# Optimization experiments

Hardware: AMD Instinct MI355X
Metric: run time of the kernel (lower is better)

The kernel has to match this reference:

```python
import jax, jax.numpy as jnp
import numpy as np


def _mlp(h, W1, b1, W2, b2):
    # Linear -> ReLU -> Linear
    h = jax.nn.relu(h @ W1 + b1)
    return h @ W2 + b2


def setup_inputs() -> dict:
    key = jax.random.key(0)
    ks = jax.random.split(key, 8)
    N, E, DN, DE, H, O = 50000, 800000, 128, 64, 256, 128
    DIN = DN + DE  # 192
    s1 = 1.0 / np.sqrt(DIN)
    s2 = 1.0 / np.sqrt(H)
    return {
        "x": jax.random.normal(ks[0], (N, DN), dtype=jnp.float32),
        "edge_index": jax.random.randint(ks[1], (2, E), 0, N, dtype=jnp.int32),
        "edge_attr": jax.random.normal(ks[2], (E, DE), dtype=jnp.float32),
        "W1_out": jax.random.normal(ks[3], (DIN, H), dtype=jnp.float32) * s1,
        "b1_out": jnp.zeros((H,), dtype=jnp.float32),
        "W2_out": jax.random.normal(ks[4], (H, O), dtype=jnp.float32) * s2,
        "b2_out": jnp.zeros((O,), dtype=jnp.float32),
        "W1_in": jax.random.normal(ks[5], (DIN, H), dtype=jnp.float32) * s1,
        "b1_in": jnp.zeros((H,), dtype=jnp.float32),
        "W2_in": jax.random.normal(ks[6], (H, O), dtype=jnp.float32) * s2,
        "b2_in": jnp.zeros((O,), dtype=jnp.float32),
    }


def reference(x, edge_index, edge_attr, W1_out, b1_out, W2_out, b2_out,
              W1_in, b1_in, W2_in, b2_in):
    N = x.shape[0]
    row, col = edge_index[0], edge_index[1]
    # Shared gather + concat: [E, d_node + d_edge]
    msg_in = jnp.concatenate([x[col], edge_attr], axis=1)

    # flow_out: edges with row < col. Compute MLP densely, zero masked edges,
    # then scatter-sum -> identical math to masked gather + scatter-sum.
    m_out = (row < col).astype(x.dtype)[:, None]
    flow_out = _mlp(msg_in, W1_out, b1_out, W2_out, b2_out) * m_out
    flow_out = jax.ops.segment_sum(flow_out, row, num_segments=N)

    # flow_in: edges with row > col
    m_in = (row > col).astype(x.dtype)[:, None]
    flow_in = _mlp(msg_in, W1_in, b1_in, W2_in, b2_in) * m_in
    flow_in = jax.ops.segment_sum(flow_in, row, num_segments=N)

    return jnp.concatenate((flow_in, flow_out), axis=1)  # [N, 2*O]
```

## Files before the change

### kernel.cpp

```cpp
#include <hip/hip_runtime.h>
#include <hip/hip_bf16.h>

typedef __attribute__((ext_vector_type(8))) short short8;
typedef __attribute__((ext_vector_type(8))) unsigned short ushort8;
typedef __attribute__((ext_vector_type(4))) float f32x4;
typedef __attribute__((ext_vector_type(2))) unsigned int uint2v;
typedef __attribute__((ext_vector_type(4))) unsigned int uint4v;

#define DN   128
#define DE   64
#define DIN  192
#define HID  256
#define OUTD 128
#define TE   64
#define NT   256
#define MSG_LD 200
#define OUT_LD 132
#define NMB  (TE / 16)

static __device__ __forceinline__ unsigned short f2b(float f) {
    unsigned int u = __float_as_uint(f);
    u += 0x7fffu + ((u >> 16) & 1u);
    return (unsigned short)(u >> 16);
}

static __device__ __forceinline__ unsigned int cvt_pk2(float lo, float hi) {
    unsigned int r;
    asm("v_cvt_pk_bf16_f32 %0, %1, %2" : "=v"(r) : "v"(lo), "v"(hi));
    return r;
}

template<int OFF>
static __device__ __forceinline__ uint2v tr_read(unsigned addr) {
    uint2v d;
    asm volatile("ds_read_b64_tr_b16 %0, %1 offset:%c2"
                 : "=v"(d) : "v"(addr), "n"(OFF));
    return d;
}

__global__ __launch_bounds__(256)
void prep_kernel(const float* __restrict__ W1o, const float* __restrict__ W1i,
                 const float* __restrict__ W2o, const float* __restrict__ W2i,
                 unsigned short* __restrict__ W1po, unsigned short* __restrict__ W1pi,
                 unsigned short* __restrict__ W2po, unsigned short* __restrict__ W2pi,
                 const int* __restrict__ ei, int E, int N, int* __restrict__ hist,
                 const float* __restrict__ x, unsigned short* __restrict__ xb) {
    const int S1 = DIN * HID, S2v = HID * OUTD;
    const int PACKN = 2 * S1 + 2 * S2v;
    int idx = blockIdx.x * blockDim.x + threadIdx.x;
    if (idx < PACKN) {
        const float* W; unsigned short* Wp; int Nc, j;
        if      (idx < S1)          { W = W1o; Wp = W1po; Nc = HID;  j = idx; }
        else if (idx < 2*S1)        { W = W1i; Wp = W1pi; Nc = HID;  j = idx - S1; }
        else if (idx < 2*S1 + S2v)  { W = W2o; Wp = W2po; Nc = OUTD; j = idx - 2*S1; }
        else                        { W = W2i; Wp = W2pi; Nc = OUTD; j = idx - 2*S1 - S2v; }
        int k = j / Nc, n = j - k * Nc;
        Wp[(((k >> 5) * Nc + n) << 5) + (k & 31)] = f2b(W[j]);
    } else if (idx < PACKN + E) {
        int e = idx - PACKN;
        int r = ei[e], c = ei[E + e];
        if      (r < c) atomicAdd(&hist[r], 1);
        else if (r > c) atomicAdd(&hist[N + r], 1);
    } else {
        int i = idx - PACKN - E;
        if (i < N * DN / 8) {
            float4 a = reinterpret_cast<const float4*>(x)[i * 2];
            float4 b = reinterpret_cast<const float4*>(x)[i * 2 + 1];
            ushort8 v = { f2b(a.x), f2b(a.y), f2b(a.z), f2b(a.w),
                          f2b(b.x), f2b(b.y), f2b(b.z), f2b(b.w) };
            reinterpret_cast<ushort8*>(xb)[i] = v;
        }
    }
}

__global__ __launch_bounds__(1024)
void scan1_kernel(const int* __restrict__ hist, int* __restrict__ cursor,
                  int* __restrict__ chunkSum, int N, int nch) {
    __shared__ int s_ws[16];
    const int br = blockIdx.x / nch, ch = blockIdx.x - br * nch;
    const int tid = threadIdx.x, lane = tid & 63, wv = tid >> 6;
    const int i = ch * 1024 + tid;
    int v = (i < N) ? hist[(size_t)br * N + i] : 0;
    int incl = v;
    #pragma unroll
    for (int d = 1; d < 64; d <<= 1) {
        int t = __shfl_up(incl, d, 64);
        if (lane >= d) incl += t;
    }
    if (lane == 63) s_ws[wv] = incl;
    __syncthreads();
    if (tid < 16) {
        int w = s_ws[tid];
        int wi = w;
        #pragma unroll
        for (int d = 1; d < 16; d <<= 1) {
            int t = __shfl_up(wi, d, 64);
            if (tid >= d) wi += t;
        }
        s_ws[tid] = wi - w;
    }
    __syncthreads();
    int excl = s_ws[wv] + incl - v;
    if (i < N) cursor[(size_t)br * N + i] = excl;
    if (tid == 1023) chunkSum[br * nch + ch] = excl + v;
}

__global__ __launch_bounds__(128)
void scan2_kernel(int* __restrict__ chunkSum, int* __restrict__ cnt, int nch) {
    const int br = threadIdx.x >> 6, lane = threadIdx.x & 63;
    int v = (lane < nch) ? chunkSum[br * nch + lane] : 0;
    int incl = v;
    #pragma unroll
    for (int d = 1; d < 64; d <<= 1) {
        int t = __shfl_up(incl, d, 64);
        if (lane >= d) incl += t;
    }
    if (lane < nch) chunkSum[br * nch + lane] = incl - v;
    if (lane == nch - 1) cnt[br] = incl;
}

__global__ __launch_bounds__(256)
void reorder_kernel(const int* __restrict__ ei, int E, int N, int nch,
                    int* __restrict__ cursor, const int* __restrict__ chunkSum,
                    int* __restrict__ list_out, int* __restrict__ list_in) {
    int e = blockIdx.x * blockDim.x + threadIdx.x;
    if (e >= E) return;
    int r = ei[e], c = ei[E + e];
    if (r == c) return;
    int br = (r < c) ? 0 : 1;
    int p = chunkSum[br * nch + (r >> 10)] + atomicAdd(&cursor[(size_t)br * N + r], 1);
    (br ? list_in : list_out)[p] = e;
}

__global__ __launch_bounds__(NT, 4)
void mlp_scatter_kernel(const unsigned short* __restrict__ xb,
                        const int* __restrict__ ei,
                        const float* __restrict__ ea,
                        const unsigned short* __restrict__ W1p_out,
                        const unsigned short* __restrict__ W1p_in,
                        const float* __restrict__ b1_out,
                        const float* __restrict__ b1_in,
                        const unsigned short* __restrict__ W2p_out,
                        const unsigned short* __restrict__ W2p_in,
                        const float* __restrict__ b2_out,
                        const float* __restrict__ b2_in,
                        const int* __restrict__ list_out,
                        const int* __restrict__ list_in,
                        const int* __restrict__ cnt,
                        float* __restrict__ out,
                        int E) {
    __shared__ __align__(16) unsigned short s_buf[TE * 264];
    __shared__ int s_eid[TE], s_dest[TE], s_col[TE];

    const int c0 = cnt[0], c1 = cnt[1];
    const int nb0 = (c0 + TE - 1) / TE;
    const int branch = (blockIdx.x >= nb0) ? 1 : 0;
    const int lb = branch ? (blockIdx.x - nb0) : blockIdx.x;
    const int count = branch ? c1 : c0;
    if (lb * TE >= count) return;
    const int* list            = branch ? list_in : list_out;
    const unsigned short* W1p  = branch ? W1p_in  : W1p_out;
    const float* b1            = branch ? b1_in   : b1_out;
    const unsigned short* W2p  = branch ? W2p_in  : W2p_out;
    const float* b2            = branch ? b2_in   : b2_out;
    const int colbase          = branch ? 0 : OUTD;

    const int tid = threadIdx.x;
    if (tid < TE) {
        int idx = lb * TE + tid;
        int e = (idx < count) ? list[idx] : -1;
        s_eid[tid]  = e;
        s_dest[tid] = (e >= 0) ? ei[e] : -1;
        s_col[tid]  = (e >= 0) ? ei[E + e] : 0;
    }
    __syncthreads();

    {
        const int le  = tid >> 2;
        const int sub = tid & 3;
        const int e   = s_eid[le];
        const ushort8* xrow = reinterpret_cast<const ushort8*>(xb) + (size_t)s_col[le] * (DN / 8);
        #pragma unroll
        for (int j = 0; j < 4; ++j) {
            int seg = sub + j * 4;
            ushort8 v = {0, 0, 0, 0, 0, 0, 0, 0};
            if (e >= 0) v = xrow[seg];
            *reinterpret_cast<ushort8*>(&s_buf[le * MSG_LD + seg * 8]) = v;
        }
        const float4* erow = reinterpret_cast<const float4*>(ea) + (size_t)e * (DE / 4);
        #pragma unroll
        for (int j = 0; j < 4; ++j) {
            float4 v = make_float4(0.f, 0.f, 0.f, 0.f);
            if (e >= 0) v = erow[sub * 4 + j];
            unsigned int lo = cvt_pk2(v.x, v.y);
            unsigned int hi = cvt_pk2(v.z, v.w);
            *reinterpret_cast<uint2*>(&s_buf[le * MSG_LD + DN + sub * 16 + j * 4]) = make_uint2(lo, hi);
        }
    }
    __syncthreads();

    const int wave = tid >> 6;
    const int lane = tid & 63;
    const int ln   = lane & 15;
    const int quad = lane >> 4;

    f32x4 acc[4][4];
    {
        const int nbase = wave * 64;
        float bias[4];
        #pragma unroll
        for (int t = 0; t < 4; ++t) bias[t] = b1[nbase + t * 16 + ln];
        #pragma unroll
        for (int mt = 0; mt < 4; ++mt)
            #pragma unroll
            for (int t = 0; t < 4; ++t)
                acc[mt][t] = (f32x4){bias[t], bias[t], bias[t], bias[t]};
        #pragma unroll
        for (int kt = 0; kt < DIN / 32; ++kt) {
            short8 a[4], b[4];
            #pragma unroll
            for (int mt = 0; mt < 4; ++mt)
                a[mt] = *reinterpret_cast<const short8*>(
                    &s_buf[(mt * 16 + ln) * MSG_LD + kt * 32 + quad * 8]);
            #pragma unroll
            for (int t = 0; t < 4; ++t)
                b[t] = *reinterpret_cast<const short8*>(
                    &W1p[((kt * HID + nbase + t * 16 + ln) << 5) + quad * 8]);
            #pragma unroll
            for (int mt = 0; mt < 4; ++mt)
                #pragma unroll
                for (int t = 0; t < 4; ++t)
                    acc[mt][t] = __builtin_amdgcn_mfma_f32_16x16x32_bf16(a[mt], b[t], acc[mt][t], 0, 0, 0);
        }
    }
    __syncthreads();

    {
        const int nbase = wave * 64;
        #pragma unroll
        for (int mt = 0; mt < 4; ++mt)
            #pragma unroll
            for (int t = 0; t < 4; ++t) {
                int n = nbase + t * 16 + ln;
                float r0 = acc[mt][t][0], r1 = acc[mt][t][1];
                float r2 = acc[mt][t][2], r3 = acc[mt][t][3];
                r0 = r0 > 0.f ? r0 : 0.f;  r1 = r1 > 0.f ? r1 : 0.f;
                r2 = r2 > 0.f ? r2 : 0.f;  r3 = r3 > 0.f ? r3 : 0.f;
                unsigned int d0 = cvt_pk2(r0, r1);
                unsigned int d1 = cvt_pk2(r2, r3);
                int el = (((n >> 2) * NMB + mt) << 6) + ((n & 3) << 4) + (quad << 2);
                *reinterpret_cast<uint2v*>(&s_buf[el]) = (uint2v){d0, d1};
            }
    }
    __syncthreads();

    f32x4 acc2[4][2];
    {
        const int nb2 = wave * 32;
        float bz0 = b2[nb2 + ln];
        float bz1 = b2[nb2 + 16 + ln];
        #pragma unroll
        for (int mt = 0; mt < 4; ++mt) {
            acc2[mt][0] = (f32x4){bz0, bz0, bz0, bz0};
            acc2[mt][1] = (f32x4){bz1, bz1, bz1, bz1};
        }
        const unsigned trb = (unsigned)(uintptr_t)(&s_buf[quad * 512 + ln * 4]);
        short8 bn0 = *reinterpret_cast<const short8*>(&W2p[((nb2 + ln) << 5) + quad * 8]);
        short8 bn1 = *reinterpret_cast<const short8*>(&W2p[((nb2 + 16 + ln) << 5) + quad * 8]);

#define G2TR(kt, mt) { \
        uint2v t0 = tr_read<(kt) * 4096 + (mt) * 128>(trb); \
        uint2v t1 = tr_read<(kt) * 4096 + (mt) * 128 + 512>(trb); \
        a[mt] = __builtin_bit_cast(short8, (uint4v){t0.x, t0.y, t1.x, t1.y}); }

#define G2MM(mt) \
        acc2[mt][0] = __builtin_amdgcn_mfma_f32_16x16x32_bf16(a[mt], b0c, acc2[mt][0], 0, 0, 0); \
        acc2[mt][1] = __builtin_amdgcn_mfma_f32_16x16x32_bf16(a[mt], b1c, acc2[mt][1], 0, 0, 0);

#define G2STEP(kt) { \
        short8 a[4]; \
        G2TR(kt, 0) G2TR(kt, 1) G2TR(kt, 2) G2TR(kt, 3) \
        short8 b0c = bn0, b1c = bn1; \
        if ((kt) < 7) { \
            bn0 = *reinterpret_cast<const short8*>(&W2p[((((kt) + 1) * OUTD + nb2 + ln) << 5) + quad * 8]); \
            bn1 = *reinterpret_cast<const short8*>(&W2p[((((kt) + 1) * OUTD + nb2 + 16 + ln) << 5) + quad * 8]); \
        } \
        asm volatile("s_waitcnt lgkmcnt(0)"); \
        __builtin_amdgcn_sched_barrier(0); \
        G2MM(0) G2MM(1) G2MM(2) G2MM(3) }

        G2STEP(0) G2STEP(1) G2STEP(2) G2STEP(3)
        G2STEP(4) G2STEP(5) G2STEP(6) G2STEP(7)
#undef G2STEP
#undef G2MM
#undef G2TR
    }
    __syncthreads();

    float* s_outf = reinterpret_cast<float*>(s_buf);
    {
        const int nb2 = wave * 32;
        #pragma unroll
        for (int mt = 0; mt < 4; ++mt)
            #pragma unroll
            for (int t = 0; t < 2; ++t)
                #pragma unroll
                for (int r = 0; r < 4; ++r)
                    s_outf[(mt * 16 + quad * 4 + r) * OUT_LD + nb2 + t * 16 + ln] = acc2[mt][t][r];
    }
    __syncthreads();

    {
        const int c  = tid & 127;
        const int m0 = (tid >> 7) * 32;
        float run = 0.f;
        int cur = -1, rs = m0;
        for (int m = m0; m < m0 + 32; ++m) {
            int d = s_dest[m];
            float v = s_outf[m * OUT_LD + c];
            if (d != cur) {
                if (cur >= 0) {
                    float* p = &out[(size_t)cur * (2 * OUTD) + colbase + c];
                    if (rs > m0) *p = run; else atomicAdd(p, run);
                }
                cur = d; run = 0.f; rs = m;
            }
            if (d >= 0) run += v;
        }
        if (cur >= 0)
            atomicAdd(&out[(size_t)cur * (2 * OUTD) + colbase + c], run);
    }
}

extern "C" void kernel_launch(void* const* d_in, const int* in_sizes, int n_in,
                              void* d_out, int out_size, void* d_ws, size_t ws_size,
                              hipStream_t stream) {
    const float* x   = (const float*)d_in[0];
    const int*   ei  = (const int*)d_in[1];
    const float* ea  = (const float*)d_in[2];
    const float* W1o = (const float*)d_in[3];
    const float* b1o = (const float*)d_in[4];
    const float* W2o = (const float*)d_in[5];
    const float* b2o = (const float*)d_in[6];
    const float* W1i = (const float*)d_in[7];
    const float* b1i = (const float*)d_in[8];
    const float* W2i = (const float*)d_in[9];
    const float* b2i = (const float*)d_in[10];
    float* out = (float*)d_out;
    const int E = in_sizes[1] / 2;
    const int N = in_sizes[0] / DN;
    const int nch = (N + 1023) >> 10;

    int* cnt      = (int*)d_ws;
    int* chunkSum = cnt + 16;
    int* hist     = chunkSum + 128;
    int* cursor   = hist + 2 * (size_t)N;
    int* list_out = cursor + 2 * (size_t)N;
    int* list_in  = list_out + E;
    unsigned short* W1po = (unsigned short*)(list_in + E);
    unsigned short* W1pi = W1po + DIN * HID;
    unsigned short* W2po = W1pi + DIN * HID;
    unsigned short* W2pi = W2po + HID * OUTD;
    unsigned short* xb   = W2pi + HID * OUTD;

    hipMemsetAsync(d_out, 0, (size_t)out_size * sizeof(float), stream);
    hipMemsetAsync(d_ws, 0, (576 + 8 * (size_t)N), stream);

    const int PACKN = 2 * DIN * HID + 2 * HID * OUTD;
    const int prepN = PACKN + E + N * DN / 8;
    prep_kernel<<<(prepN + 255) / 256, 256, 0, stream>>>(
        W1o, W1i, W2o, W2i, W1po, W1pi, W2po, W2pi, ei, E, N, hist, x, xb);

    scan1_kernel<<<2 * nch, 1024, 0, stream>>>(hist, cursor, chunkSum, N, nch);
    scan2_kernel<<<1, 128, 0, stream>>>(chunkSum, cnt, nch);
    reorder_kernel<<<(E + 255) / 256, 256, 0, stream>>>(
        ei, E, N, nch, cursor, chunkSum, list_out, list_in);

    const int nblk = (E + TE - 1) / TE + 2;
    mlp_scatter_kernel<<<nblk, NT, 0, stream>>>(
        xb, ei, ea, W1po, W1pi, b1o, b1i, W2po, W2pi, b2o, b2i,
        list_out, list_in, cnt, out, E);
}
```

Baseline: 573.7 us.

## Precompute per-node first-layer projection and gather it instead of raw node features

Result: slower. 622.2 us (+8.5%).

```diff
diff --git a/kernel.cpp b/kernel.cpp
--- a/kernel.cpp
+++ b/kernel.cpp
@@ -14,7 +14,9 @@
 #define OUTD 128
 #define TE   64
 #define NT   256
-#define MSG_LD 200
+#define EA_LD 72
+#define Z_LD  264
+#define ZX_LD 136
 #define OUT_LD 132
 #define NMB  (TE / 16)
 
@@ -43,8 +45,7 @@
                  const float* __restrict__ W2o, const float* __restrict__ W2i,
                  unsigned short* __restrict__ W1po, unsigned short* __restrict__ W1pi,
                  unsigned short* __restrict__ W2po, unsigned short* __restrict__ W2pi,
-                 const int* __restrict__ ei, int E, int N, int* __restrict__ hist,
-                 const float* __restrict__ x, unsigned short* __restrict__ xb) {
+                 const int* __restrict__ ei, int E, int N, int* __restrict__ hist) {
     const int S1 = DIN * HID, S2v = HID * OUTD;
     const int PACKN = 2 * S1 + 2 * S2v;
     int idx = blockIdx.x * blockDim.x + threadIdx.x;
@@ -61,14 +62,92 @@
         int r = ei[e], c = ei[E + e];
         if      (r < c) atomicAdd(&hist[r], 1);
         else if (r > c) atomicAdd(&hist[N + r], 1);
-    } else {
-        int i = idx - PACKN - E;
-        if (i < N * DN / 8) {
-            float4 a = reinterpret_cast<const float4*>(x)[i * 2];
-            float4 b = reinterpret_cast<const float4*>(x)[i * 2 + 1];
-            ushort8 v = { f2b(a.x), f2b(a.y), f2b(a.z), f2b(a.w),
-                          f2b(b.x), f2b(b.y), f2b(b.z), f2b(b.w) };
-            reinterpret_cast<ushort8*>(xb)[i] = v;
+    }
+}
+
+__global__ __launch_bounds__(256, 4)
+void z_kernel(const float* __restrict__ x,
+              const unsigned short* __restrict__ W1p_out,
+              const unsigned short* __restrict__ W1p_in,
+              const float* __restrict__ b1_out, const float* __restrict__ b1_in,
+              unsigned short* __restrict__ z, int N) {
+    __shared__ __align__(16) unsigned short s_t[64 * Z_LD];
+    const int nzb = (N + 63) >> 6;
+    const int branch = (blockIdx.x >= nzb) ? 1 : 0;
+    const int zb = blockIdx.x - branch * nzb;
+    const unsigned short* W1p = branch ? W1p_in : W1p_out;
+    const float* b1           = branch ? b1_in  : b1_out;
+    const int r0 = zb * 64;
+    const int tid = threadIdx.x;
+
+    {
+        const int row = tid >> 2, sub = tid & 3;
+        const float* xr = x + (size_t)(r0 + row) * DN + sub * 32;
+        const bool ok = (r0 + row) < N;
+        #pragma unroll
+        for (int j = 0; j < 4; ++j) {
+            float4 a = make_float4(0.f, 0.f, 0.f, 0.f), b = a;
+            if (ok) {
+                a = *reinterpret_cast<const float4*>(xr + j * 8);
+                b = *reinterpret_cast<const float4*>(xr + j * 8 + 4);
+            }
+            uint4v v = { cvt_pk2(a.x, a.y), cvt_pk2(a.z, a.w),
+                         cvt_pk2(b.x, b.y), cvt_pk2(b.z, b.w) };
+            *reinterpret_cast<uint4v*>(&s_t[row * ZX_LD + sub * 32 + j * 8]) = v;
+        }
+    }
+    __syncthreads();
+
+    const int wave = tid >> 6, lane = tid & 63, ln = lane & 15, quad = lane >> 4;
+    const int nbase = wave * 64;
+    f32x4 acc[4][4];
+    {
+        float bias[4];
+        #pragma unroll
+        for (int t = 0; t < 4; ++t) bias[t] = b1[nbase + t * 16 + ln];
+        #pragma unroll
+        for (int mt = 0; mt < 4; ++mt)
+            #pragma unroll
+            for (int t = 0; t < 4; ++t)
+                acc[mt][t] = (f32x4){bias[t], bias[t], bias[t], bias[t]};
+        #pragma unroll
+        for (int kt = 0; kt < DN / 32; ++kt) {
+            short8 a[4], b[4];
+            #pragma unroll
+            for (int mt = 0; mt < 4; ++mt)
+                a[mt] = *reinterpret_cast<const short8*>(
+                    &s_t[(mt * 16 + ln) * ZX_LD + kt * 32 + quad * 8]);
+            #pragma unroll
+            for (int t = 0; t < 4; ++t)
+                b[t] = *reinterpret_cast<const short8*>(
+                    &W1p[((kt * HID + nbase + t * 16 + ln) << 5) + quad * 8]);
+            #pragma unroll
+            for (int mt = 0; mt < 4; ++mt)
+                #pragma unroll
+                for (int t = 0; t < 4; ++t)
+                    acc[mt][t] = __builtin_amdgcn_mfma_f32_16x16x32_bf16(a[mt], b[t], acc[mt][t], 0, 0, 0);
+        }
+    }
+    __syncthreads();
+
+    #pragma unroll
+    for (int mt = 0; mt < 4; ++mt)
+        #pragma unroll
+        for (int t = 0; t < 4; ++t) {
+            int n = nbase + t * 16 + ln;
+            #pragma unroll
+            for (int r = 0; r < 4; ++r)
+                s_t[(mt * 16 + quad * 4 + r) * Z_LD + n] = f2b(acc[mt][t][r]);
+        }
+    __syncthreads();
+
+    {
+        unsigned short* zg = z + (size_t)branch * N * HID;
+        for (int c = tid; c < 64 * 32; c += NT) {
+            int row = c >> 5, ch = c & 31;
+            if (r0 + row < N)
+                reinterpret_cast<ushort8*>(zg + (size_t)(r0 + row) * HID)[ch] =
+                    *reinterpret_cast<const ushort8*>(&s_t[row * Z_LD + ch * 8]);
         }
     }
 }
@@ -132,14 +211,12 @@
     (br ? list_in : list_out)[p] = e;
 }
 
-__global__ __launch_bounds__(NT, 4)
-void mlp_scatter_kernel(const unsigned short* __restrict__ xb,
+__global__ __launch_bounds__(NT, 3)
+void mlp_scatter_kernel(const unsigned short* __restrict__ z,
                         const int* __restrict__ ei,
                         const float* __restrict__ ea,
                         const unsigned short* __restrict__ W1p_out,
                         const unsigned short* __restrict__ W1p_in,
-                        const float* __restrict__ b1_out,
-                        const float* __restrict__ b1_in,
                         const unsigned short* __restrict__ W2p_out,
                         const unsigned short* __restrict__ W2p_in,
                         const float* __restrict__ b2_out,
@@ -148,8 +225,9 @@
                         const int* __restrict__ list_in,
                         const int* __restrict__ cnt,
                         float* __restrict__ out,
-                        int E) {
-    __shared__ __align__(16) unsigned short s_buf[TE * 264];
+                        int E, int N) {
+    __shared__ __align__(16) unsigned short s_buf[TE * Z_LD];
+    __shared__ __align__(16) unsigned short s_msg[TE * EA_LD];
     __shared__ int s_eid[TE], s_dest[TE], s_col[TE];
 
     const int c0 = cnt[0], c1 = cnt[1];
@@ -160,7 +238,6 @@
     if (lb * TE >= count) return;
     const int* list            = branch ? list_in : list_out;
     const unsigned short* W1p  = branch ? W1p_in  : W1p_out;
-    const float* b1            = branch ? b1_in   : b1_out;
     const unsigned short* W2p  = branch ? W2p_in  : W2p_out;
     const float* b2            = branch ? b2_in   : b2_out;
     const int colbase          = branch ? 0 : OUTD;
@@ -179,13 +256,14 @@
         const int le  = tid >> 2;
         const int sub = tid & 3;
         const int e   = s_eid[le];
-        const ushort8* xrow = reinterpret_cast<const ushort8*>(xb) + (size_t)s_col[le] * (DN / 8);
-        #pragma unroll
-        for (int j = 0; j < 4; ++j) {
-            int seg = sub + j * 4;
+        const ushort8* zrow = reinterpret_cast<const ushort8*>(z)
+            + ((size_t)branch * N + s_col[le]) * (HID / 8);
+        #pragma unroll
+        for (int j = 0; j < 8; ++j) {
+            int seg = j * 4 + sub;
             ushort8 v = {0, 0, 0, 0, 0, 0, 0, 0};
-            if (e >= 0) v = xrow[seg];
-            *reinterpret_cast<ushort8*>(&s_buf[le * MSG_LD + seg * 8]) = v;
+            if (e >= 0) v = zrow[seg];
+            *reinterpret_cast<ushort8*>(&s_buf[le * Z_LD + seg * 8]) = v;
         }
         const float4* erow = reinterpret_cast<const float4*>(ea) + (size_t)e * (DE / 4);
         #pragma unroll
@@ -194,7 +272,7 @@
             if (e >= 0) v = erow[sub * 4 + j];
             unsigned int lo = cvt_pk2(v.x, v.y);
             unsigned int hi = cvt_pk2(v.z, v.w);
-            *reinterpret_cast<uint2*>(&s_buf[le * MSG_LD + DN + sub * 16 + j * 4]) = make_uint2(lo, hi);
+            *reinterpret_cast<uint2*>(&s_msg[le * EA_LD + sub * 16 + j * 4]) = make_uint2(lo, hi);
         }
     }
     __syncthreads();
@@ -207,25 +285,29 @@
     f32x4 acc[4][4];
     {
         const int nbase = wave * 64;
-        float bias[4];
-        #pragma unroll
-        for (int t = 0; t < 4; ++t) bias[t] = b1[nbase + t * 16 + ln];
         #pragma unroll
         for (int mt = 0; mt < 4; ++mt)
             #pragma unroll
-            for (int t = 0; t < 4; ++t)
-                acc[mt][t] = (f32x4){bias[t], bias[t], bias[t], bias[t]};
-        #pragma unroll
-        for (int kt = 0; kt < DIN / 32; ++kt) {
+            for (int t = 0; t < 4; ++t) {
+                int n = nbase + t * 16 + ln;
+                #pragma unroll
+                for (int r = 0; r < 4; ++r) {
+                    int m = mt * 16 + quad * 4 + r;
+                    acc[mt][t][r] = __uint_as_float(
+                        (unsigned int)s_buf[m * Z_LD + n] << 16);
+                }
+            }
+        #pragma unroll
+        for (int kt = 0; kt < DE / 32; ++kt) {
             short8 a[4], b[4];
             #pragma unroll
             for (int mt = 0; mt < 4; ++mt)
                 a[mt] = *reinterpret_cast<const short8*>(
-                    &s_buf[(mt * 16 + ln) * MSG_LD + kt * 32 + quad * 8]);
+                    &s_msg[(mt * 16 + ln) * EA_LD + kt * 32 + quad * 8]);
             #pragma unroll
             for (int t = 0; t < 4; ++t)
                 b[t] = *reinterpret_cast<const short8*>(
-                    &W1p[((kt * HID + nbase + t * 16 + ln) << 5) + quad * 8]);
+                    &W1p[(((kt + DN / 32) * HID + nbase + t * 16 + ln) << 5) + quad * 8]);
             #pragma unroll
             for (int mt = 0; mt < 4; ++mt)
                 #pragma unroll
@@ -361,15 +443,23 @@
     unsigned short* W1pi = W1po + DIN * HID;
     unsigned short* W2po = W1pi + DIN * HID;
     unsigned short* W2pi = W2po + HID * OUTD;
-    unsigned short* xb   = W2pi + HID * OUTD;
+    unsigned short* zws  = W2pi + HID * OUTD;
+
+    size_t need = (size_t)(144 + 4 * (size_t)N + 2 * (size_t)E) * 4
+                + (size_t)(2 * DIN * HID + 2 * HID * OUTD) * 2
+                + (size_t)2 * N * HID * 2;
+    if (need > ws_size) return;
 
     hipMemsetAsync(d_out, 0, (size_t)out_size * sizeof(float), stream);
     hipMemsetAsync(d_ws, 0, (576 + 8 * (size_t)N), stream);
 
     const int PACKN = 2 * DIN * HID + 2 * HID * OUTD;
-    const int prepN = PACKN + E + N * DN / 8;
+    const int prepN = PACKN + E;
     prep_kernel<<<(prepN + 255) / 256, 256, 0, stream>>>(
-        W1o, W1i, W2o, W2i, W1po, W1pi, W2po, W2pi, ei, E, N, hist, x, xb);
+        W1o, W1i, W2o, W2i, W1po, W1pi, W2po, W2pi, ei, E, N, hist);
+
+    const int nzb = (N + 63) >> 6;
+    z_kernel<<<2 * nzb, 256, 0, stream>>>(x, W1po, W1pi, b1o, b1i, zws, N);
 
     scan1_kernel<<<2 * nch, 1024, 0, stream>>>(hist, cursor, chunkSum, N, nch);
     scan2_kernel<<<1, 128, 0, stream>>>(chunkSum, cnt, nch);
@@ -378,6 +468,6 @@
 
     const int nblk = (E + TE - 1) / TE + 2;
     mlp_scatter_kernel<<<nblk, NT, 0, stream>>>(
-        xb, ei, ea, W1po, W1pi, b1o, b1i, W2po, W2pi, b2o, b2i,
-        list_out, list_in, cnt, out, E);
-}
+        zws, ei, ea, W1po, W1pi, W2po, W2pi, b2o, b2i,
+        list_out, list_in, cnt, out, E, N);
+}
```

## Load x operands directly from global, overlap edge_attr staging, double-buffer GEMM2 reads

Applied to the files above, without the earlier changes.

Result: slower. 627.0 us (+9.3%).

```diff
diff --git a/kernel.cpp b/kernel.cpp
--- a/kernel.cpp
+++ b/kernel.cpp
@@ -14,7 +14,7 @@
 #define OUTD 128
 #define TE   64
 #define NT   256
-#define MSG_LD 200
+#define EA_LD 72
 #define OUT_LD 132
 #define NMB  (TE / 16)
 
@@ -175,35 +175,22 @@
     }
     __syncthreads();
 
-    {
-        const int le  = tid >> 2;
-        const int sub = tid & 3;
-        const int e   = s_eid[le];
-        const ushort8* xrow = reinterpret_cast<const ushort8*>(xb) + (size_t)s_col[le] * (DN / 8);
-        #pragma unroll
-        for (int j = 0; j < 4; ++j) {
-            int seg = sub + j * 4;
-            ushort8 v = {0, 0, 0, 0, 0, 0, 0, 0};
-            if (e >= 0) v = xrow[seg];
-            *reinterpret_cast<ushort8*>(&s_buf[le * MSG_LD + seg * 8]) = v;
-        }
-        const float4* erow = reinterpret_cast<const float4*>(ea) + (size_t)e * (DE / 4);
-        #pragma unroll
-        for (int j = 0; j < 4; ++j) {
-            float4 v = make_float4(0.f, 0.f, 0.f, 0.f);
-            if (e >= 0) v = erow[sub * 4 + j];
-            unsigned int lo = cvt_pk2(v.x, v.y);
-            unsigned int hi = cvt_pk2(v.z, v.w);
-            *reinterpret_cast<uint2*>(&s_buf[le * MSG_LD + DN + sub * 16 + j * 4]) = make_uint2(lo, hi);
-        }
-    }
-    __syncthreads();
-
     const int wave = tid >> 6;
     const int lane = tid & 63;
     const int ln   = lane & 15;
     const int quad = lane >> 4;
 
+    const int le  = tid >> 2;
+    const int sub = tid & 3;
+    const int eg  = s_eid[le];
+    float4 ev[4];
+    {
+        const float4* erow = reinterpret_cast<const float4*>(ea)
+            + (size_t)(eg < 0 ? 0 : eg) * (DE / 4);
+        #pragma unroll
+        for (int j = 0; j < 4; ++j) ev[j] = erow[sub * 4 + j];
+    }
+
     f32x4 acc[4][4];
     {
         const int nbase = wave * 64;
@@ -215,17 +202,53 @@
             #pragma unroll
             for (int t = 0; t < 4; ++t)
                 acc[mt][t] = (f32x4){bias[t], bias[t], bias[t], bias[t]};
-        #pragma unroll
-        for (int kt = 0; kt < DIN / 32; ++kt) {
+
+        const unsigned short* xp0 = xb + (size_t)s_col[0 * 16 + ln] * DN + quad * 8;
+        const unsigned short* xp1 = xb + (size_t)s_col[1 * 16 + ln] * DN + quad * 8;
+        const unsigned short* xp2 = xb + (size_t)s_col[2 * 16 + ln] * DN + quad * 8;
+        const unsigned short* xp3 = xb + (size_t)s_col[3 * 16 + ln] * DN + quad * 8;
+        #pragma unroll
+        for (int kt = 0; kt < DN / 32; ++kt) {
             short8 a[4], b[4];
-            #pragma unroll
-            for (int mt = 0; mt < 4; ++mt)
-                a[mt] = *reinterpret_cast<const short8*>(
-                    &s_buf[(mt * 16 + ln) * MSG_LD + kt * 32 + quad * 8]);
+            a[0] = *reinterpret_cast<const short8*>(xp0 + kt * 32);
+            a[1] = *reinterpret_cast<const short8*>(xp1 + kt * 32);
+            a[2] = *reinterpret_cast<const short8*>(xp2 + kt * 32);
+            a[3] = *reinterpret_cast<const short8*>(xp3 + kt * 32);
             #pragma unroll
             for (int t = 0; t < 4; ++t)
                 b[t] = *reinterpret_cast<const short8*>(
                     &W1p[((kt * HID + nbase + t * 16 + ln) << 5) + quad * 8]);
+            #pragma unroll
+            for (int mt = 0; mt < 4; ++mt)
+                #pragma unroll
+                for (int t = 0; t < 4; ++t)
+                    acc[mt][t] = __builtin_amdgcn_mfma_f32_16x16x32_bf16(a[mt], b[t], acc[mt][t], 0, 0, 0);
+        }
+    }
+
+    {
+        #pragma unroll
+        for (int j = 0; j < 4; ++j) {
+            unsigned int lo = cvt_pk2(ev[j].x, ev[j].y);
+            unsigned int hi = cvt_pk2(ev[j].z, ev[j].w);
+            *reinterpret_cast<uint2*>(&s_buf[le * EA_LD + sub * 16 + j * 4]) = make_uint2(lo, hi);
+        }
+    }
+    __syncthreads();
+
+    {
+        const int nbase = wave * 64;
+        #pragma unroll
+        for (int kk = 0; kk < DE / 32; ++kk) {
+            short8 a[4], b[4];
+            #pragma unroll
+            for (int mt = 0; mt < 4; ++mt)
+                a[mt] = *reinterpret_cast<const short8*>(
+                    &s_buf[(mt * 16 + ln) * EA_LD + kk * 32 + quad * 8]);
+            #pragma unroll
+            for (int t = 0; t < 4; ++t)
+                b[t] = *reinterpret_cast<const short8*>(
+                    &W1p[(((kk + DN / 32) * HID + nbase + t * 16 + ln) << 5) + quad * 8]);
             #pragma unroll
             for (int mt = 0; mt < 4; ++mt)
                 #pragma unroll
@@ -268,32 +291,52 @@
         short8 bn0 = *reinterpret_cast<const short8*>(&W2p[((nb2 + ln) << 5) + quad * 8]);
         short8 bn1 = *reinterpret_cast<const short8*>(&W2p[((nb2 + 16 + ln) << 5) + quad * 8]);
 
-#define G2TR(kt, mt) { \
-        uint2v t0 = tr_read<(kt) * 4096 + (mt) * 128>(trb); \
-        uint2v t1 = tr_read<(kt) * 4096 + (mt) * 128 + 512>(trb); \
-        a[mt] = __builtin_bit_cast(short8, (uint4v){t0.x, t0.y, t1.x, t1.y}); }
-
-#define G2MM(mt) \
-        acc2[mt][0] = __builtin_amdgcn_mfma_f32_16x16x32_bf16(a[mt], b0c, acc2[mt][0], 0, 0, 0); \
-        acc2[mt][1] = __builtin_amdgcn_mfma_f32_16x16x32_bf16(a[mt], b1c, acc2[mt][1], 0, 0, 0);
-
-#define G2STEP(kt) { \
-        short8 a[4]; \
-        G2TR(kt, 0) G2TR(kt, 1) G2TR(kt, 2) G2TR(kt, 3) \
+#define G2LOAD(dst, kt) { \
+        uint2v u0 = tr_read<(kt) * 4096 + 0 * 128>(trb); \
+        uint2v u1 = tr_read<(kt) * 4096 + 0 * 128 + 512>(trb); \
+        uint2v u2 = tr_read<(kt) * 4096 + 1 * 128>(trb); \
+        uint2v u3 = tr_read<(kt) * 4096 + 1 * 128 + 512>(trb); \
+        uint2v u4 = tr_read<(kt) * 4096 + 2 * 128>(trb); \
+        uint2v u5 = tr_read<(kt) * 4096 + 2 * 128 + 512>(trb); \
+        uint2v u6 = tr_read<(kt) * 4096 + 3 * 128>(trb); \
+        uint2v u7 = tr_read<(kt) * 4096 + 3 * 128 + 512>(trb); \
+        dst[0] = __builtin_bit_cast(short8, (uint4v){u0.x, u0.y, u1.x, u1.y}); \
+        dst[1] = __builtin_bit_cast(short8, (uint4v){u2.x, u2.y, u3.x, u3.y}); \
+        dst[2] = __builtin_bit_cast(short8, (uint4v){u4.x, u4.y, u5.x, u5.y}); \
+        dst[3] = __builtin_bit_cast(short8, (uint4v){u6.x, u6.y, u7.x, u7.y}); }
+
+#define G2WAIT8 { asm volatile("s_waitcnt lgkmcnt(8)"); __builtin_amdgcn_sched_barrier(0); }
+#define G2WAIT0 { asm volatile("s_waitcnt lgkmcnt(0)"); __builtin_amdgcn_sched_barrier(0); }
+
+#define G2MMA(src, kt) { \
         short8 b0c = bn0, b1c = bn1; \
         if ((kt) < 7) { \
             bn0 = *reinterpret_cast<const short8*>(&W2p[((((kt) + 1) * OUTD + nb2 + ln) << 5) + quad * 8]); \
             bn1 = *reinterpret_cast<const short8*>(&W2p[((((kt) + 1) * OUTD + nb2 + 16 + ln) << 5) + quad * 8]); \
         } \
-        asm volatile("s_waitcnt lgkmcnt(0)"); \
-        __builtin_amdgcn_sched_barrier(0); \
-        G2MM(0) G2MM(1) G2MM(2) G2MM(3) }
-
-        G2STEP(0) G2STEP(1) G2STEP(2) G2STEP(3)
-        G2STEP(4) G2STEP(5) G2STEP(6) G2STEP(7)
-#undef G2STEP
-#undef G2MM
-#undef G2TR
+        acc2[0][0] = __builtin_amdgcn_mfma_f32_16x16x32_bf16(src[0], b0c, acc2[0][0], 0, 0, 0); \
+        acc2[0][1] = __builtin_amdgcn_mfma_f32_16x16x32_bf16(src[0], b1c, acc2[0][1], 0, 0, 0); \
+        acc2[1][0] = __builtin_amdgcn_mfma_f32_16x16x32_bf16(src[1], b0c, acc2[1][0], 0, 0, 0); \
+        acc2[1][1] = __builtin_amdgcn_mfma_f32_16x16x32_bf16(src[1], b1c, acc2[1][1], 0, 0, 0); \
+        acc2[2][0] = __builtin_amdgcn_mfma_f32_16x16x32_bf16(src[2], b0c, acc2[2][0], 0, 0, 0); \
+        acc2[2][1] = __builtin_amdgcn_mfma_f32_16x16x32_bf16(src[2], b1c, acc2[2][1], 0, 0, 0); \
+        acc2[3][0] = __builtin_amdgcn_mfma_f32_16x16x32_bf16(src[3], b0c, acc2[3][0], 0, 0, 0); \
+        acc2[3][1] = __builtin_amdgcn_mfma_f32_16x16x32_bf16(src[3], b1c, acc2[3][1], 0, 0, 0); }
+
+        short8 aA[4], aB[4];
+        G2LOAD(aA, 0)
+        G2LOAD(aB, 1) G2WAIT8 G2MMA(aA, 0)
+        G2LOAD(aA, 2) G2WAIT8 G2MMA(aB, 1)
+        G2LOAD(aB, 3) G2WAIT8 G2MMA(aA, 2)
+        G2LOAD(aA, 4) G2WAIT8 G2MMA(aB, 3)
+        G2LOAD(aB, 5) G2WAIT8 G2MMA(aA, 4)
+        G2LOAD(aA, 6) G2WAIT8 G2MMA(aB, 5)
+        G2LOAD(aB, 7) G2WAIT8 G2MMA(aA, 6)
+                      G2WAIT0 G2MMA(aB, 7)
+#undef G2MMA
+#undef G2WAIT8
+#undef G2WAIT0
+#undef G2LOAD
     }
     __syncthreads();
 
@@ -363,6 +406,11 @@
     unsigned short* W2pi = W2po + HID * OUTD;
     unsigned short* xb   = W2pi + HID * OUTD;
 
+    size_t need = (size_t)(144 + 4 * (size_t)N + 2 * (size_t)E) * 4
+                + (size_t)(2 * DIN * HID + 2 * HID * OUTD) * 2
+                + (size_t)N * DN * 2;
+    if (need > ws_size) return;
+
     hipMemsetAsync(d_out, 0, (size_t)out_size * sizeof(float), stream);
     hipMemsetAsync(d_ws, 0, (576 + 8 * (size_t)N), stream);
 
```

## Repartition second GEMM by edge rows per wave and pipeline LDS transpose reads

Applied to the files above, without the earlier changes.

New measurement: 655.8 us. +14.3%, slower.

```diff
diff --git a/kernel.cpp b/kernel.cpp
--- a/kernel.cpp
+++ b/kernel.cpp
@@ -49,13 +49,21 @@
     const int PACKN = 2 * S1 + 2 * S2v;
     int idx = blockIdx.x * blockDim.x + threadIdx.x;
     if (idx < PACKN) {
-        const float* W; unsigned short* Wp; int Nc, j;
-        if      (idx < S1)          { W = W1o; Wp = W1po; Nc = HID;  j = idx; }
-        else if (idx < 2*S1)        { W = W1i; Wp = W1pi; Nc = HID;  j = idx - S1; }
-        else if (idx < 2*S1 + S2v)  { W = W2o; Wp = W2po; Nc = OUTD; j = idx - 2*S1; }
-        else                        { W = W2i; Wp = W2pi; Nc = OUTD; j = idx - 2*S1 - S2v; }
-        int k = j / Nc, n = j - k * Nc;
-        Wp[(((k >> 5) * Nc + n) << 5) + (k & 31)] = f2b(W[j]);
+        if (idx < 2 * S1) {
+            const float* W = (idx < S1) ? W1o : W1i;
+            unsigned short* Wp = (idx < S1) ? W1po : W1pi;
+            int j = (idx < S1) ? idx : idx - S1;
+            int k5 = j & 31, t = j >> 5;
+            int n = t & (HID - 1), kq = t >> 8;
+            Wp[j] = f2b(W[(kq * 32 + k5) * HID + n]);
+        } else {
+            const float* W = (idx < 2 * S1 + S2v) ? W2o : W2i;
+            unsigned short* Wp = (idx < 2 * S1 + S2v) ? W2po : W2pi;
+            int j = (idx < 2 * S1 + S2v) ? idx - 2 * S1 : idx - 2 * S1 - S2v;
+            int k5 = j & 31, t = j >> 5;
+            int n = t & (OUTD - 1), kq = t >> 7;
+            Wp[j] = f2b(W[(kq * 32 + k5) * OUTD + n]);
+        }
     } else if (idx < PACKN + E) {
         int e = idx - PACKN;
         int r = ei[e], c = ei[E + e];
@@ -189,12 +197,12 @@
         }
         const float4* erow = reinterpret_cast<const float4*>(ea) + (size_t)e * (DE / 4);
         #pragma unroll
-        for (int j = 0; j < 4; ++j) {
-            float4 v = make_float4(0.f, 0.f, 0.f, 0.f);
-            if (e >= 0) v = erow[sub * 4 + j];
-            unsigned int lo = cvt_pk2(v.x, v.y);
-            unsigned int hi = cvt_pk2(v.z, v.w);
-            *reinterpret_cast<uint2*>(&s_buf[le * MSG_LD + DN + sub * 16 + j * 4]) = make_uint2(lo, hi);
+        for (int jj = 0; jj < 2; ++jj) {
+            float4 v0 = make_float4(0.f, 0.f, 0.f, 0.f), v1 = v0;
+            if (e >= 0) { v0 = erow[sub * 4 + jj * 2]; v1 = erow[sub * 4 + jj * 2 + 1]; }
+            uint4v w = { cvt_pk2(v0.x, v0.y), cvt_pk2(v0.z, v0.w),
+                         cvt_pk2(v1.x, v1.y), cvt_pk2(v1.z, v1.w) };
+            *reinterpret_cast<uint4v*>(&s_buf[le * MSG_LD + DN + sub * 16 + jj * 8]) = w;
         }
     }
     __syncthreads();
@@ -254,59 +262,54 @@
     }
     __syncthreads();
 
-    f32x4 acc2[4][2];
-    {
-        const int nb2 = wave * 32;
-        float bz0 = b2[nb2 + ln];
-        float bz1 = b2[nb2 + 16 + ln];
-        #pragma unroll
-        for (int mt = 0; mt < 4; ++mt) {
-            acc2[mt][0] = (f32x4){bz0, bz0, bz0, bz0};
-            acc2[mt][1] = (f32x4){bz1, bz1, bz1, bz1};
-        }
-        const unsigned trb = (unsigned)(uintptr_t)(&s_buf[quad * 512 + ln * 4]);
-        short8 bn0 = *reinterpret_cast<const short8*>(&W2p[((nb2 + ln) << 5) + quad * 8]);
-        short8 bn1 = *reinterpret_cast<const short8*>(&W2p[((nb2 + 16 + ln) << 5) + quad * 8]);
-
-#define G2TR(kt, mt) { \
-        uint2v t0 = tr_read<(kt) * 4096 + (mt) * 128>(trb); \
-        uint2v t1 = tr_read<(kt) * 4096 + (mt) * 128 + 512>(trb); \
-        a[mt] = __builtin_bit_cast(short8, (uint4v){t0.x, t0.y, t1.x, t1.y}); }
-
-#define G2MM(mt) \
-        acc2[mt][0] = __builtin_amdgcn_mfma_f32_16x16x32_bf16(a[mt], b0c, acc2[mt][0], 0, 0, 0); \
-        acc2[mt][1] = __builtin_amdgcn_mfma_f32_16x16x32_bf16(a[mt], b1c, acc2[mt][1], 0, 0, 0);
-
-#define G2STEP(kt) { \
-        short8 a[4]; \
-        G2TR(kt, 0) G2TR(kt, 1) G2TR(kt, 2) G2TR(kt, 3) \
-        short8 b0c = bn0, b1c = bn1; \
-        if ((kt) < 7) { \
-            bn0 = *reinterpret_cast<const short8*>(&W2p[((((kt) + 1) * OUTD + nb2 + ln) << 5) + quad * 8]); \
-            bn1 = *reinterpret_cast<const short8*>(&W2p[((((kt) + 1) * OUTD + nb2 + 16 + ln) << 5) + quad * 8]); \
-        } \
-        asm volatile("s_waitcnt lgkmcnt(0)"); \
+    f32x4 acc2[8];
+    {
+        #pragma unroll
+        for (int t = 0; t < 8; ++t) {
+            float bz = b2[t * 16 + ln];
+            acc2[t] = (f32x4){bz, bz, bz, bz};
+        }
+        const unsigned trb = (unsigned)(uintptr_t)(&s_buf[quad * 512 + wave * 64 + ln * 4]);
+
+#define G2ISSUE(kt) \
+        uint2v t0_##kt = tr_read<(kt) * 4096>(trb); \
+        uint2v t1_##kt = tr_read<(kt) * 4096 + 512>(trb);
+
+#define G2BODY(kt, WAITN) { \
+        short8 b[8]; \
+        _Pragma("unroll") \
+        for (int t = 0; t < 8; ++t) \
+            b[t] = *reinterpret_cast<const short8*>( \
+                &W2p[(((kt) * OUTD + t * 16 + ln) << 5) + quad * 8]); \
+        asm volatile("s_waitcnt lgkmcnt(" #WAITN ")"); \
         __builtin_amdgcn_sched_barrier(0); \
-        G2MM(0) G2MM(1) G2MM(2) G2MM(3) }
-
-        G2STEP(0) G2STEP(1) G2STEP(2) G2STEP(3)
-        G2STEP(4) G2STEP(5) G2STEP(6) G2STEP(7)
-#undef G2STEP
-#undef G2MM
-#undef G2TR
+        short8 a = __builtin_bit_cast(short8, \
+            (uint4v){t0_##kt.x, t0_##kt.y, t1_##kt.x, t1_##kt.y}); \
+        _Pragma("unroll") \
+        for (int t = 0; t < 8; ++t) \
+            acc2[t] = __builtin_amdgcn_mfma_f32_16x16x32_bf16(a, b[t], acc2[t], 0, 0, 0); }
+
+        G2ISSUE(0)
+        G2ISSUE(1) G2BODY(0, 2)
+        G2ISSUE(2) G2BODY(1, 2)
+        G2ISSUE(3) G2BODY(2, 2)
+        G2ISSUE(4) G2BODY(3, 2)
+        G2ISSUE(5) G2BODY(4, 2)
+        G2ISSUE(6) G2BODY(5, 2)
+        G2ISSUE(7) G2BODY(6, 2)
+                   G2BODY(7, 0)
+#undef G2BODY
+#undef G2ISSUE
     }
     __syncthreads();
 
     float* s_outf = reinterpret_cast<float*>(s_buf);
     {
-        const int nb2 = wave * 32;
-        #pragma unroll
-        for (int mt = 0; mt < 4; ++mt)
-            #pragma unroll
-            for (int t = 0; t < 2; ++t)
-                #pragma unroll
-                for (int r = 0; r < 4; ++r)
-                    s_outf[(mt * 16 + quad * 4 + r) * OUT_LD + nb2 + t * 16 + ln] = acc2[mt][t][r];
+        #pragma unroll
+        for (int t = 0; t < 8; ++t)
+            #pragma unroll
+            for (int r = 0; r < 4; ++r)
+                s_outf[(wave * 16 + quad * 4 + r) * OUT_LD + t * 16 + ln] = acc2[t][r];
     }
     __syncthreads();
 
@@ -363,6 +366,11 @@
     unsigned short* W2pi = W2po + HID * OUTD;
     unsigned short* xb   = W2pi + HID * OUTD;
 
+    size_t need = (size_t)(144 + 4 * (size_t)N + 2 * (size_t)E) * 4
+                + (size_t)(2 * DIN * HID + 2 * HID * OUTD) * 2
+                + (size_t)N * DN * 2;
+    if (need > ws_size) return;
+
     hipMemsetAsync(d_out, 0, (size_t)out_size * sizeof(float), stream);
     hipMemsetAsync(d_ws, 0, (576 + 8 * (size_t)N), stream);
 
```
